# Optimization experiments

Hardware: AMD Instinct MI355X
Metric: run time of the kernel (lower is better)

Reference implementation:

```python
import jax, jax.numpy as jnp
import numpy as np

B, T, E, H = 2, 256, 512, 8
D = E // H  # head_dim = 64 (even)


def setup_inputs() -> dict:
    key = jax.random.key(0)
    ks = jax.random.split(key, 4)
    x = jax.random.normal(ks[0], (B, T, E), jnp.float32)
    # pairwise complex rotary mask, stored as (..., 2) = (real, imag)
    attn_mask = jax.random.normal(ks[1], (B, 1, T, T, D // 2, 2), jnp.float32)
    pad_mask = jnp.zeros((B, 1, 1, T), jnp.float32)
    Wqkv = jax.random.normal(ks[2], (E, 3 * E), jnp.float32) * (E ** -0.5)
    bqkv = jnp.zeros((3 * E,), jnp.float32)
    Wo = jax.random.normal(ks[3], (E, E), jnp.float32) * (E ** -0.5)
    bo = jnp.zeros((E,), jnp.float32)
    return {"x": x, "attn_mask": attn_mask, "pad_mask": pad_mask,
            "Wqkv": Wqkv, "bqkv": bqkv, "Wo": Wo, "bo": bo}


def reference(x, attn_mask, pad_mask, Wqkv, bqkv, Wo, bo):
    scale = 1.0 / np.sqrt(D)
    qkv = x @ Wqkv + bqkv                                   # (B,T,3E)
    q, k, v = jnp.split(qkv, 3, axis=-1)
    q = q.reshape(B, T, H, D).transpose(0, 2, 1, 3)         # (B,H,T,D)
    v = v.reshape(B, T, H, D).transpose(0, 2, 1, 3)         # (B,H,S,D)
    # keys as complex pairs: (B,H,1,S,D/2,2)
    k = k.reshape(B, T, H, D // 2, 2).transpose(0, 2, 1, 3, 4)[:, :, None]
    m = attn_mask                                           # (B,1,T,S,D/2,2)
    # complex multiply k * m -> rotated keys per (query, key) pair
    kr = k[..., 0] * m[..., 0] - k[..., 1] * m[..., 1]      # (B,H,T,S,D/2)
    ki = k[..., 0] * m[..., 1] + k[..., 1] * m[..., 0]
    krot = jnp.stack([kr, ki], axis=-1).reshape(B, H, T, T, D)
    a = jnp.einsum('bhtd,bhtsd->bhts', q, krot) * scale     # (B,H,T,S)
    a = a + pad_mask
    a = jax.nn.softmax(a, axis=-1)
    # (eval mode: no dropout)
    o = jnp.einsum('bhts,bhsd->bhtd', a, v)                 # (B,H,T,D)
    o = o.transpose(0, 2, 1, 3).reshape(B, T, E)
    o = o @ Wo + bo
    attn_weights = a.sum(axis=1) / H                        # (B,T,S)
    return o, attn_weights
```

## Files before the change

### kernel.cpp

```cpp
#include <hip/hip_runtime.h>
#include <math.h>

#define Bb 2
#define Tt 256
#define Ee 512
#define Hh 8
#define Dd 64
#define E3 1536
#define SCP 260

typedef float vfloat4 __attribute__((ext_vector_type(4)));
typedef short bf16x8 __attribute__((ext_vector_type(8)));
typedef float f32x4 __attribute__((ext_vector_type(4)));

__device__ inline float4 ntload4(const float* p) {
    vfloat4 v = __builtin_nontemporal_load((const vfloat4*)p);
    return make_float4(v.x, v.y, v.z, v.w);
}
template<int CTRL>
__device__ inline float dpp_addf(float v) {
    int x = __builtin_amdgcn_update_dpp(0, __float_as_int(v), CTRL, 0xF, 0xF, true);
    return v + __int_as_float(x);
}
__device__ inline float swz4_addf(float v) {
    int x = __builtin_amdgcn_ds_swizzle(__float_as_int(v), 0x101F);
    return v + __int_as_float(x);
}
__device__ inline unsigned short bf16rne(float f) {
    unsigned u = __float_as_uint(f);
    return (unsigned short)((u + 0x7FFFu + ((u >> 16) & 1u)) >> 16);
}
__device__ inline float bf16tof(unsigned short h) {
    return __uint_as_float(((unsigned)h) << 16);
}
__device__ inline bf16x8 ldb(const unsigned short* p) {
    return *(const bf16x8*)(const void*)p;
}
__device__ __forceinline__ void split8(const float* p, bf16x8& hi, bf16x8& lo) {
    const float4 a = *(const float4*)p, b = *(const float4*)(p + 4);
    float f[8] = {a.x, a.y, a.z, a.w, b.x, b.y, b.z, b.w};
    bf16x8 h, l;
    #pragma unroll
    for (int i = 0; i < 8; ++i) {
        const unsigned short hh = bf16rne(f[i]);
        h[i] = (short)hh;
        l[i] = (short)bf16rne(f[i] - bf16tof(hh));
    }
    hi = h; lo = l;
}
__device__ __forceinline__ f32x4 mfma3(f32x4 acc, bf16x8 ah, bf16x8 al,
                                       bf16x8 bh, bf16x8 bl) {
    acc = __builtin_amdgcn_mfma_f32_16x16x32_bf16(ah, bh, acc, 0, 0, 0);
    acc = __builtin_amdgcn_mfma_f32_16x16x32_bf16(al, bh, acc, 0, 0, 0);
    acc = __builtin_amdgcn_mfma_f32_16x16x32_bf16(ah, bl, acc, 0, 0, 0);
    return acc;
}

__global__ __launch_bounds__(256) void prep_w(
    const float* __restrict__ Wqkv, const float* __restrict__ Wo,
    unsigned short* __restrict__ Wqhi, unsigned short* __restrict__ Wqlo,
    unsigned short* __restrict__ Wohi, unsigned short* __restrict__ Wolo)
{
    __shared__ float tile[64][65];
    const int bid = blockIdx.x, tid = threadIdx.x;
    const float* src; unsigned short *dhi, *dlo; int Nw, kt, nt;
    if (bid < 192) { src = Wqkv; dhi = Wqhi; dlo = Wqlo; Nw = 1536; kt = bid & 7; nt = bid >> 3; }
    else { const int b2 = bid - 192; src = Wo; dhi = Wohi; dlo = Wolo; Nw = 512; kt = b2 & 7; nt = b2 >> 3; }
    const int rr = tid >> 2, cc = (tid & 3) * 16;
    #pragma unroll
    for (int j = 0; j < 4; ++j) {
        const float4 v = *(const float4*)&src[(size_t)(kt * 64 + rr) * Nw + nt * 64 + cc + j * 4];
        tile[rr][cc + j * 4 + 0] = v.x;
        tile[rr][cc + j * 4 + 1] = v.y;
        tile[rr][cc + j * 4 + 2] = v.z;
        tile[rr][cc + j * 4 + 3] = v.w;
    }
    __syncthreads();
    unsigned short hb[16], lb[16];
    #pragma unroll
    for (int j = 0; j < 16; ++j) {
        const float f = tile[cc + j][rr];
        const unsigned short h = bf16rne(f);
        hb[j] = h;
        lb[j] = bf16rne(f - bf16tof(h));
    }
    const size_t off = (size_t)(nt * 64 + rr) * 512 + kt * 64 + cc;
    *(uint4*)&dhi[off]     = *(const uint4*)&hb[0];
    *(uint4*)&dhi[off + 8] = *(const uint4*)&hb[8];
    *(uint4*)&dlo[off]     = *(const uint4*)&lb[0];
    *(uint4*)&dlo[off + 8] = *(const uint4*)&lb[8];
}

__global__ __launch_bounds__(256) void mfma_qkv(
    const float* __restrict__ x,
    const unsigned short* __restrict__ Bhi, const unsigned short* __restrict__ Blo,
    const float* __restrict__ bias, float* __restrict__ C, int M, int N)
{
    __shared__ f32x4 red[4][2][2][64];
    const int lane = threadIdx.x & 63;
    const int wv   = threadIdx.x >> 6;
    const int m0   = blockIdx.y * 32;
    const int n0   = blockIdx.x * 32;
    const int fr   = lane & 15;
    const int kg   = (lane >> 4) * 8;

    f32x4 acc00 = {0.f, 0.f, 0.f, 0.f}, acc01 = acc00, acc10 = acc00, acc11 = acc00;

    #pragma unroll
    for (int s = 0; s < 4; ++s) {
        const int k0 = wv * 128 + s * 32 + kg;
        bf16x8 ah0, al0, ah1, al1;
        split8(&x[(size_t)(m0 + fr) * 512 + k0], ah0, al0);
        split8(&x[(size_t)(m0 + 16 + fr) * 512 + k0], ah1, al1);
        const bf16x8 bh0 = ldb(Bhi + (size_t)(n0 + fr) * 512 + k0);
        const bf16x8 bl0 = ldb(Blo + (size_t)(n0 + fr) * 512 + k0);
        const bf16x8 bh1 = ldb(Bhi + (size_t)(n0 + 16 + fr) * 512 + k0);
        const bf16x8 bl1 = ldb(Blo + (size_t)(n0 + 16 + fr) * 512 + k0);
        acc00 = mfma3(acc00, ah0, al0, bh0, bl0);
        acc01 = mfma3(acc01, ah0, al0, bh1, bl1);
        acc10 = mfma3(acc10, ah1, al1, bh0, bl0);
        acc11 = mfma3(acc11, ah1, al1, bh1, bl1);
    }
    red[wv][0][0][lane] = acc00;
    red[wv][0][1][lane] = acc01;
    red[wv][1][0][lane] = acc10;
    red[wv][1][1][lane] = acc11;
    __syncthreads();

    const int fi = wv >> 1, fj = wv & 1;
    f32x4 s0 = red[0][fi][fj][lane];
    const f32x4 s1 = red[1][fi][fj][lane];
    const f32x4 s2 = red[2][fi][fj][lane];
    const f32x4 s3 = red[3][fi][fj][lane];
    #pragma unroll
    for (int g = 0; g < 4; ++g) s0[g] = (s0[g] + s1[g]) + (s2[g] + s3[g]);
    const int dr = (lane >> 4) * 4, dc = lane & 15;
    const float bs = bias[n0 + fj * 16 + dc];
    #pragma unroll
    for (int g = 0; g < 4; ++g)
        C[(size_t)(m0 + fi * 16 + dr + g) * N + n0 + fj * 16 + dc] = s0[g] + bs;
}

__global__ __launch_bounds__(256) void mfma_proj(
    const unsigned short* __restrict__ Ahi, const unsigned short* __restrict__ Alo,
    const unsigned short* __restrict__ Bhi, const unsigned short* __restrict__ Blo,
    const float* __restrict__ bias, float* __restrict__ C, int M, int N)
{
    __shared__ f32x4 red[4][2][2][64];
    const int lane = threadIdx.x & 63;
    const int wv   = threadIdx.x >> 6;
    const int m0   = blockIdx.y * 32;
    const int n0   = blockIdx.x * 32;
    const int fr   = lane & 15;
    const int kg   = (lane >> 4) * 8;

    f32x4 acc00 = {0.f, 0.f, 0.f, 0.f}, acc01 = acc00, acc10 = acc00, acc11 = acc00;

    #pragma unroll
    for (int s = 0; s < 4; ++s) {
        const int k0 = wv * 128 + s * 32 + kg;
        const bf16x8 ah0 = ldb(Ahi + (size_t)(m0 + fr) * 512 + k0);
        const bf16x8 al0 = ldb(Alo + (size_t)(m0 + fr) * 512 + k0);
        const bf16x8 ah1 = ldb(Ahi + (size_t)(m0 + 16 + fr) * 512 + k0);
        const bf16x8 al1 = ldb(Alo + (size_t)(m0 + 16 + fr) * 512 + k0);
        const bf16x8 bh0 = ldb(Bhi + (size_t)(n0 + fr) * 512 + k0);
        const bf16x8 bl0 = ldb(Blo + (size_t)(n0 + fr) * 512 + k0);
        const bf16x8 bh1 = ldb(Bhi + (size_t)(n0 + 16 + fr) * 512 + k0);
        const bf16x8 bl1 = ldb(Blo + (size_t)(n0 + 16 + fr) * 512 + k0);
        acc00 = mfma3(acc00, ah0, al0, bh0, bl0);
        acc01 = mfma3(acc01, ah0, al0, bh1, bl1);
        acc10 = mfma3(acc10, ah1, al1, bh0, bl0);
        acc11 = mfma3(acc11, ah1, al1, bh1, bl1);
    }
    red[wv][0][0][lane] = acc00;
    red[wv][0][1][lane] = acc01;
    red[wv][1][0][lane] = acc10;
    red[wv][1][1][lane] = acc11;
    __syncthreads();

    const int fi = wv >> 1, fj = wv & 1;
    f32x4 s0 = red[0][fi][fj][lane];
    const f32x4 s1 = red[1][fi][fj][lane];
    const f32x4 s2 = red[2][fi][fj][lane];
    const f32x4 s3 = red[3][fi][fj][lane];
    #pragma unroll
    for (int g = 0; g < 4; ++g) s0[g] = (s0[g] + s1[g]) + (s2[g] + s3[g]);
    const int dr = (lane >> 4) * 4, dc = lane & 15;
    const float bs = bias[n0 + fj * 16 + dc];
    #pragma unroll
    for (int g = 0; g < 4; ++g)
        C[(size_t)(m0 + fi * 16 + dr + g) * N + n0 + fj * 16 + dc] = s0[g] + bs;
}

__global__ __launch_bounds__(512, 2) void attn_kernel(
    const float* __restrict__ qkv, const float* __restrict__ mask,
    const float* __restrict__ pad,
    unsigned short* __restrict__ oahi, unsigned short* __restrict__ oalo,
    float* __restrict__ attn_w)
{
    __shared__ float sc[2][Hh][SCP];
    __shared__ float part[4][2][Hh][68];
    __shared__ float rrs[16];
    const int tid  = threadIdx.x;
    const int lane = tid & 63;
    const int wv   = tid >> 6;
    const int si   = lane >> 3;
    const int dq   = lane & 7;
    const int b    = blockIdx.x >> 7;
    const int t0   = (blockIdx.x & 127) * 2;

    float4 qr[2][Hh][2];
    {
        const float* qb = qkv + (size_t)(b * Tt + t0) * E3 + dq * 8;
        #pragma unroll
        for (int t = 0; t < 2; ++t)
            #pragma unroll
            for (int h = 0; h < Hh; ++h) {
                qr[t][h][0] = *(const float4*)(qb + (size_t)t * E3 + h * 64);
                qr[t][h][1] = *(const float4*)(qb + (size_t)t * E3 + h * 64 + 4);
            }
    }
    const float scale = 0.125f;

    const float* mbase0 = mask + (size_t)(b * Tt + t0) * Tt * Dd + dq * 8;
    const float* mbase1 = mbase0 + (size_t)Tt * Dd;
    float4 mc[2][4];
    {
        const int s0 = wv * 32 + si;
        const float* m0p = mbase0 + (size_t)s0 * Dd;
        const float* m1p = mbase1 + (size_t)s0 * Dd;
        mc[0][0] = ntload4(m0p); mc[0][1] = ntload4(m0p + 4);
        mc[0][2] = ntload4(m1p); mc[0][3] = ntload4(m1p + 4);
    }
    #pragma unroll
    for (int c = 0; c < 4; ++c) {
        const int s = wv * 32 + c * 8 + si;
        const int cb = c & 1, nbm = cb ^ 1;
        if (c < 3) {
            const int sn = s + 8;
            const float* m0p = mbase0 + (size_t)sn * Dd;
            const float* m1p = mbase1 + (size_t)sn * Dd;
            mc[nbm][0] = ntload4(m0p); mc[nbm][1] = ntload4(m0p + 4);
            mc[nbm][2] = ntload4(m1p); mc[nbm][3] = ntload4(m1p + 4);
        }
        const float4 ma0 = mc[cb][0], mb0 = mc[cb][1];
        const float4 ma1 = mc[cb][2], mb1 = mc[cb][3];
        const float* krow = qkv + (size_t)(b * Tt + s) * E3 + Ee + dq * 8;
        const float padv = pad[b * Tt + s];
        float4 kc[2][2];
        kc[0][0] = *(const float4*)(krow);
        kc[0][1] = *(const float4*)(krow + 4);
        #pragma unroll
        for (int h = 0; h < Hh; ++h) {
            const int hb = h & 1, hn = hb ^ 1;
            if (h < 7) {
                kc[hn][0] = *(const float4*)(krow + (h + 1) * 64);
                kc[hn][1] = *(const float4*)(krow + (h + 1) * 64 + 4);
            }
            const float4 ka = kc[hb][0], kb = kc[hb][1];
            const float4 qa0 = qr[0][h][0], qb0 = qr[0][h][1];
            const float4 qa1 = qr[1][h][0], qb1 = qr[1][h][1];
            float u0 = qa0.x * ka.x + qa0.y * ka.y;
            float w0 = qa0.y * ka.x - qa0.x * ka.y;
            float u1 = qa0.z * ka.z + qa0.w * ka.w;
            float w1 = qa0.w * ka.z - qa0.z * ka.w;
            float u2 = qb0.x * kb.x + qb0.y * kb.y;
            float w2 = qb0.y * kb.x - qb0.x * kb.y;
            float u3 = qb0.z * kb.z + qb0.w * kb.w;
            float w3 = qb0.w * kb.z - qb0.z * kb.w;
            float v0 = u0 * ma0.x + w0 * ma0.y + u1 * ma0.z + w1 * ma0.w
                     + u2 * mb0.x + w2 * mb0.y + u3 * mb0.z + w3 * mb0.w;
            float s0 = qa1.x * ka.x + qa1.y * ka.y;
            float r0 = qa1.y * ka.x - qa1.x * ka.y;
            float s1 = qa1.z * ka.z + qa1.w * ka.w;
            float r1 = qa1.w * ka.z - qa1.z * ka.w;
            float s2 = qb1.x * kb.x + qb1.y * kb.y;
            float r2 = qb1.y * kb.x - qb1.x * kb.y;
            float s3 = qb1.z * kb.z + qb1.w * kb.w;
            float r3 = qb1.w * kb.z - qb1.z * kb.w;
            float v1 = s0 * ma1.x + r0 * ma1.y + s1 * ma1.z + r1 * ma1.w
                     + s2 * mb1.x + r2 * mb1.y + s3 * mb1.z + r3 * mb1.w;
            v0 = dpp_addf<0xB1>(v0); v0 = dpp_addf<0x4E>(v0); v0 = swz4_addf(v0);
            v1 = dpp_addf<0xB1>(v1); v1 = dpp_addf<0x4E>(v1); v1 = swz4_addf(v1);
            if (dq == 0) {
                sc[0][h][s] = v0 * scale + padv;
                sc[1][h][s] = v1 * scale + padv;
            }
        }
    }
    __syncthreads();

    #pragma unroll
    for (int r = 0; r < 2; ++r) {
        const int row = wv * 2 + r;
        float* pr = &sc[0][0][0] + row * SCP;
        float4 xv = *(const float4*)&pr[lane * 4];
        float mx = fmaxf(fmaxf(xv.x, xv.y), fmaxf(xv.z, xv.w));
        #pragma unroll
        for (int dlt = 32; dlt >= 1; dlt >>= 1) mx = fmaxf(mx, __shfl_xor(mx, dlt));
        float4 ev;
        ev.x = __expf(xv.x - mx);
        ev.y = __expf(xv.y - mx);
        ev.z = __expf(xv.z - mx);
        ev.w = __expf(xv.w - mx);
        float sum = (ev.x + ev.y) + (ev.z + ev.w);
        #pragma unroll
        for (int dlt = 32; dlt >= 1; dlt >>= 1) sum += __shfl_xor(sum, dlt);
        *(float4*)&pr[lane * 4] = ev;
        if (lane == 0) rrs[row] = 1.0f / sum;
    }
    __syncthreads();

    {
        const int tt = tid >> 8, s2 = tid & 255;
        float aw = 0.f;
        #pragma unroll
        for (int h = 0; h < Hh; ++h) aw += sc[tt][h][s2] * rrs[tt * 8 + h];
        attn_w[(size_t)(b * Tt + t0 + tt) * Tt + s2] = aw * 0.125f;
    }

    {
        const int sh = tid >> 7;
        const int h  = (tid >> 4) & 7;
        const int d4 = tid & 15;
        const float* vb = qkv + (size_t)b * Tt * E3 + 2 * Ee + h * 64 + d4 * 4;
        float4 o0 = make_float4(0.f, 0.f, 0.f, 0.f);
        float4 o1 = make_float4(0.f, 0.f, 0.f, 0.f);
        const int sBeg = sh * 64;
        float4 vc[2][4];
        #pragma unroll
        for (int i = 0; i < 4; ++i)
            vc[0][i] = *(const float4*)(vb + (size_t)(sBeg + i) * E3);
        #pragma unroll
        for (int it = 0; it < 16; ++it) {
            const int s2 = sBeg + it * 4;
            const int cb = it & 1, nbv = cb ^ 1;
            if (it < 15) {
                #pragma unroll
                for (int i = 0; i < 4; ++i)
                    vc[nbv][i] = *(const float4*)(vb + (size_t)(s2 + 4 + i) * E3);
            }
            const float4 p0 = *(const float4*)&sc[0][h][s2];
            const float4 p1 = *(const float4*)&sc[1][h][s2];
            const float4 va = vc[cb][0], vbv = vc[cb][1], vcv = vc[cb][2], vd = vc[cb][3];
            o0.x = fmaf(p0.x, va.x, o0.x);  o0.y = fmaf(p0.x, va.y, o0.y);
            o0.z = fmaf(p0.x, va.z, o0.z);  o0.w = fmaf(p0.x, va.w, o0.w);
            o0.x = fmaf(p0.y, vbv.x, o0.x); o0.y = fmaf(p0.y, vbv.y, o0.y);
            o0.z = fmaf(p0.y, vbv.z, o0.z); o0.w = fmaf(p0.y, vbv.w, o0.w);
            o0.x = fmaf(p0.z, vcv.x, o0.x); o0.y = fmaf(p0.z, vcv.y, o0.y);
            o0.z = fmaf(p0.z, vcv.z, o0.z); o0.w = fmaf(p0.z, vcv.w, o0.w);
            o0.x = fmaf(p0.w, vd.x, o0.x);  o0.y = fmaf(p0.w, vd.y, o0.y);
            o0.z = fmaf(p0.w, vd.z, o0.z);  o0.w = fmaf(p0.w, vd.w, o0.w);
            o1.x = fmaf(p1.x, va.x, o1.x);  o1.y = fmaf(p1.x, va.y, o1.y);
            o1.z = fmaf(p1.x, va.z, o1.z);  o1.w = fmaf(p1.x, va.w, o1.w);
            o1.x = fmaf(p1.y, vbv.x, o1.x); o1.y = fmaf(p1.y, vbv.y, o1.y);
            o1.z = fmaf(p1.y, vbv.z, o1.z); o1.w = fmaf(p1.y, vbv.w, o1.w);
            o1.x = fmaf(p1.z, vcv.x, o1.x); o1.y = fmaf(p1.z, vcv.y, o1.y);
            o1.z = fmaf(p1.z, vcv.z, o1.z); o1.w = fmaf(p1.z, vcv.w, o1.w);
            o1.x = fmaf(p1.w, vd.x, o1.x);  o1.y = fmaf(p1.w, vd.y, o1.y);
            o1.z = fmaf(p1.w, vd.z, o1.z);  o1.w = fmaf(p1.w, vd.w, o1.w);
        }
        *(float4*)&part[sh][0][h][d4 * 4] = o0;
        *(float4*)&part[sh][1][h][d4 * 4] = o1;
    }
    __syncthreads();

    {
        const int t  = tid >> 8;
        const int n2 = tid & 255;
        const int h  = n2 >> 5;
        const int dc = (2 * n2) & 63;
        const float rr = rrs[t * 8 + h];
        float ax = 0.f, ay = 0.f;
        #pragma unroll
        for (int s = 0; s < 4; ++s) {
            const float2 p = *(const float2*)&part[s][t][h][dc];
            ax += p.x; ay += p.y;
        }
        const float ox = ax * rr, oy = ay * rr;
        const unsigned short hx = bf16rne(ox), hy = bf16rne(oy);
        const unsigned short lx = bf16rne(ox - bf16tof(hx));
        const unsigned short ly = bf16rne(oy - bf16tof(hy));
        const size_t off = (size_t)(b * Tt + t0 + t) * Ee + 2 * n2;
        *(unsigned*)&oahi[off] = (unsigned)hx | ((unsigned)hy << 16);
        *(unsigned*)&oalo[off] = (unsigned)lx | ((unsigned)ly << 16);
    }
}

extern "C" void kernel_launch(void* const* d_in, const int* in_sizes, int n_in,
                              void* d_out, int out_size, void* d_ws, size_t ws_size,
                              hipStream_t stream) {
    const float* x    = (const float*)d_in[0];
    const float* mask = (const float*)d_in[1];
    const float* pad  = (const float*)d_in[2];
    const float* Wqkv = (const float*)d_in[3];
    const float* bqkv = (const float*)d_in[4];
    const float* Wo   = (const float*)d_in[5];
    const float* bo   = (const float*)d_in[6];

    float* out = (float*)d_out;

    unsigned short* Wqhi = (unsigned short*)d_ws;
    unsigned short* Wqlo = Wqhi + 786432;
    unsigned short* Wohi = Wqlo + 786432;
    unsigned short* Wolo = Wohi + 262144;
    unsigned short* oahi = Wolo + 262144;
    unsigned short* oalo = oahi + 262144;
    float* qkv = (float*)(oalo + 262144);

    prep_w<<<256, 256, 0, stream>>>(Wqkv, Wo, Wqhi, Wqlo, Wohi, Wolo);

    mfma_qkv<<<dim3(E3 / 32, (Bb * Tt) / 32), 256, 0, stream>>>(
        x, Wqhi, Wqlo, bqkv, qkv, Bb * Tt, E3);

    attn_kernel<<<dim3(Bb * (Tt / 2)), 512, 0, stream>>>(
        qkv, mask, pad, oahi, oalo, out + (size_t)Bb * Tt * Ee);

    mfma_proj<<<dim3(Ee / 32, (Bb * Tt) / 32), 256, 0, stream>>>(
        oahi, oalo, Wohi, Wolo, bo, out, Bb * Tt, Ee);
}
```

Before: 54.10 us.

## Fuse weight prep into QKV GEMM and split Wqkv on the fly

Removes the separate prep_w kernel: the QKV GEMM now reads fp32 Wqkv directly with strided scalar loads and splits it into bf16 hi/lo in registers. The Wo split runs as 64 extra blocks of the same launch. This saves one kernel launch and the round-trip of the Wqkv hi/lo buffers through memory. In exchange, each GEMM block does uncoalesced column reads of Wqkv and repeats the split work across the 16 M-tiles.

```diff
diff --git a/kernel.cpp b/kernel.cpp
--- a/kernel.cpp
+++ b/kernel.cpp
@@ -48,6 +48,16 @@
     }
     hi = h; lo = l;
 }
+__device__ __forceinline__ void split8a(const float* f, bf16x8& hi, bf16x8& lo) {
+    bf16x8 h, l;
+    #pragma unroll
+    for (int i = 0; i < 8; ++i) {
+        const unsigned short hh = bf16rne(f[i]);
+        h[i] = (short)hh;
+        l[i] = (short)bf16rne(f[i] - bf16tof(hh));
+    }
+    hi = h; lo = l;
+}
 __device__ __forceinline__ f32x4 mfma3(f32x4 acc, bf16x8 ah, bf16x8 al,
                                        bf16x8 bh, bf16x8 bl) {
     acc = __builtin_amdgcn_mfma_f32_16x16x32_bf16(ah, bh, acc, 0, 0, 0);
@@ -56,51 +66,50 @@
     return acc;
 }
 
-__global__ __launch_bounds__(256) void prep_w(
-    const float* __restrict__ Wqkv, const float* __restrict__ Wo,
-    unsigned short* __restrict__ Wqhi, unsigned short* __restrict__ Wqlo,
+__global__ __launch_bounds__(256) void mfma_qkv2(
+    const float* __restrict__ x, const float* __restrict__ Wqkv,
+    const float* __restrict__ bias, float* __restrict__ C,
+    const float* __restrict__ Wo,
     unsigned short* __restrict__ Wohi, unsigned short* __restrict__ Wolo)
 {
-    __shared__ float tile[64][65];
-    const int bid = blockIdx.x, tid = threadIdx.x;
-    const float* src; unsigned short *dhi, *dlo; int Nw, kt, nt;
-    if (bid < 192) { src = Wqkv; dhi = Wqhi; dlo = Wqlo; Nw = 1536; kt = bid & 7; nt = bid >> 3; }
-    else { const int b2 = bid - 192; src = Wo; dhi = Wohi; dlo = Wolo; Nw = 512; kt = b2 & 7; nt = b2 >> 3; }
-    const int rr = tid >> 2, cc = (tid & 3) * 16;
-    #pragma unroll
-    for (int j = 0; j < 4; ++j) {
-        const float4 v = *(const float4*)&src[(size_t)(kt * 64 + rr) * Nw + nt * 64 + cc + j * 4];
-        tile[rr][cc + j * 4 + 0] = v.x;
-        tile[rr][cc + j * 4 + 1] = v.y;
-        tile[rr][cc + j * 4 + 2] = v.z;
-        tile[rr][cc + j * 4 + 3] = v.w;
-    }
-    __syncthreads();
-    unsigned short hb[16], lb[16];
-    #pragma unroll
-    for (int j = 0; j < 16; ++j) {
-        const float f = tile[cc + j][rr];
-        const unsigned short h = bf16rne(f);
-        hb[j] = h;
-        lb[j] = bf16rne(f - bf16tof(h));
-    }
-    const size_t off = (size_t)(nt * 64 + rr) * 512 + kt * 64 + cc;
-    *(uint4*)&dhi[off]     = *(const uint4*)&hb[0];
-    *(uint4*)&dhi[off + 8] = *(const uint4*)&hb[8];
-    *(uint4*)&dlo[off]     = *(const uint4*)&lb[0];
-    *(uint4*)&dlo[off + 8] = *(const uint4*)&lb[8];
-}
-
-__global__ __launch_bounds__(256) void mfma_qkv(
-    const float* __restrict__ x,
-    const unsigned short* __restrict__ Bhi, const unsigned short* __restrict__ Blo,
-    const float* __restrict__ bias, float* __restrict__ C, int M, int N)
-{
+    const int bid = blockIdx.x;
+    const int tid = threadIdx.x;
+
+    if (bid >= 768) {
+        __shared__ float tile[64][65];
+        const int b2 = bid - 768;
+        const int kt = b2 & 7, nt = b2 >> 3;
+        const int rr = tid >> 2, cc = (tid & 3) * 16;
+        #pragma unroll
+        for (int j = 0; j < 4; ++j) {
+            const float4 v = *(const float4*)&Wo[(size_t)(kt * 64 + rr) * 512 + nt * 64 + cc + j * 4];
+            tile[rr][cc + j * 4 + 0] = v.x;
+            tile[rr][cc + j * 4 + 1] = v.y;
+            tile[rr][cc + j * 4 + 2] = v.z;
+            tile[rr][cc + j * 4 + 3] = v.w;
+        }
+        __syncthreads();
+        unsigned short hb[16], lb[16];
+        #pragma unroll
+        for (int j = 0; j < 16; ++j) {
+            const float f = tile[cc + j][rr];
+            const unsigned short h = bf16rne(f);
+            hb[j] = h;
+            lb[j] = bf16rne(f - bf16tof(h));
+        }
+        const size_t off = (size_t)(nt * 64 + rr) * 512 + kt * 64 + cc;
+        *(uint4*)&Wohi[off]     = *(const uint4*)&hb[0];
+        *(uint4*)&Wohi[off + 8] = *(const uint4*)&hb[8];
+        *(uint4*)&Wolo[off]     = *(const uint4*)&lb[0];
+        *(uint4*)&Wolo[off + 8] = *(const uint4*)&lb[8];
+        return;
+    }
+
     __shared__ f32x4 red[4][2][2][64];
-    const int lane = threadIdx.x & 63;
-    const int wv   = threadIdx.x >> 6;
-    const int m0   = blockIdx.y * 32;
-    const int n0   = blockIdx.x * 32;
+    const int lane = tid & 63;
+    const int wv   = tid >> 6;
+    const int n0   = (bid % 48) * 32;
+    const int m0   = (bid / 48) * 32;
     const int fr   = lane & 15;
     const int kg   = (lane >> 4) * 8;
 
@@ -112,10 +121,15 @@
         bf16x8 ah0, al0, ah1, al1;
         split8(&x[(size_t)(m0 + fr) * 512 + k0], ah0, al0);
         split8(&x[(size_t)(m0 + 16 + fr) * 512 + k0], ah1, al1);
-        const bf16x8 bh0 = ldb(Bhi + (size_t)(n0 + fr) * 512 + k0);
-        const bf16x8 bl0 = ldb(Blo + (size_t)(n0 + fr) * 512 + k0);
-        const bf16x8 bh1 = ldb(Bhi + (size_t)(n0 + 16 + fr) * 512 + k0);
-        const bf16x8 bl1 = ldb(Blo + (size_t)(n0 + 16 + fr) * 512 + k0);
+        float b0[8], b1[8];
+        #pragma unroll
+        for (int j = 0; j < 8; ++j) {
+            b0[j] = Wqkv[(size_t)(k0 + j) * E3 + n0 + fr];
+            b1[j] = Wqkv[(size_t)(k0 + j) * E3 + n0 + 16 + fr];
+        }
+        bf16x8 bh0, bl0, bh1, bl1;
+        split8a(b0, bh0, bl0);
+        split8a(b1, bh1, bl1);
         acc00 = mfma3(acc00, ah0, al0, bh0, bl0);
         acc01 = mfma3(acc01, ah0, al0, bh1, bl1);
         acc10 = mfma3(acc10, ah1, al1, bh0, bl0);
@@ -138,7 +152,7 @@
     const float bs = bias[n0 + fj * 16 + dc];
     #pragma unroll
     for (int g = 0; g < 4; ++g)
-        C[(size_t)(m0 + fi * 16 + dr + g) * N + n0 + fj * 16 + dc] = s0[g] + bs;
+        C[(size_t)(m0 + fi * 16 + dr + g) * E3 + n0 + fj * 16 + dc] = s0[g] + bs;
 }
 
 __global__ __launch_bounds__(256) void mfma_proj(
@@ -400,18 +414,13 @@
 
     float* out = (float*)d_out;
 
-    unsigned short* Wqhi = (unsigned short*)d_ws;
-    unsigned short* Wqlo = Wqhi + 786432;
-    unsigned short* Wohi = Wqlo + 786432;
+    unsigned short* Wohi = (unsigned short*)d_ws;
     unsigned short* Wolo = Wohi + 262144;
     unsigned short* oahi = Wolo + 262144;
     unsigned short* oalo = oahi + 262144;
     float* qkv = (float*)(oalo + 262144);
 
-    prep_w<<<256, 256, 0, stream>>>(Wqkv, Wo, Wqhi, Wqlo, Wohi, Wolo);
-
-    mfma_qkv<<<dim3(E3 / 32, (Bb * Tt) / 32), 256, 0, stream>>>(
-        x, Wqhi, Wqlo, bqkv, qkv, Bb * Tt, E3);
+    mfma_qkv2<<<832, 256, 0, stream>>>(x, Wqkv, bqkv, qkv, Wo, Wohi, Wolo);
 
     attn_kernel<<<dim3(Bb * (Tt / 2)), 512, 0, stream>>>(
         qkv, mask, pad, oahi, oalo, out + (size_t)Bb * Tt * Ee);
```

After: 46.65 us, median of 3. -13.8%, faster.
